# Kernel tuning notes

Measured on AMD Instinct MI355X. Metric: run time of the kernel, lower is better.

## Reference

```python
import jax, jax.numpy as jnp
import numpy as np

HEADS = 4
DIM_HEAD = 64
SCALE = 8.0
EPS = 1e-5  # fp32 branch of the original LayerNorm


def setup_inputs() -> dict:
    key = jax.random.key(0)
    k1, k2, k3 = jax.random.split(key, 3)
    B, C, F, H, W = 2, 256, 4, 32, 32
    inner = HEADS * DIM_HEAD  # 256
    x = jax.random.normal(k1, (B, C, F, H, W), dtype=jnp.float32)
    gamma = jnp.ones((1, C, 1, 1, 1), dtype=jnp.float32)
    w_qkv = jax.random.normal(k2, (3 * inner, C), dtype=jnp.float32) * 0.05
    w_out = jax.random.normal(k3, (C, inner), dtype=jnp.float32) * 0.05
    return {"x": x, "gamma": gamma, "w_qkv": w_qkv, "w_out": w_out}


def _l2norm(t):
    return t / jnp.sqrt(jnp.sum(t * t, axis=-1, keepdims=True) + 1e-12)


def reference(x, gamma, w_qkv, w_out):
    B, C, F, H, W = x.shape
    N = F * H * W
    inner = HEADS * DIM_HEAD
    residual = x

    # channel LayerNorm (biased variance over dim=1)
    mean = jnp.mean(x, axis=1, keepdims=True)
    var = jnp.mean((x - mean) ** 2, axis=1, keepdims=True)
    xn = (x - mean) / jnp.sqrt(var + EPS) * gamma

    # 1x1x1 conv == channel matmul; flatten spatial dims to sequence
    xn_flat = xn.reshape(B, C, N)                      # [B, C, N]
    qkv = jnp.einsum('oc,bcn->bon', w_qkv, xn_flat)    # [B, 3*inner, N]
    qkv = qkv.reshape(B, 3, HEADS, DIM_HEAD, N)        # chunk then split heads
    qkv = jnp.transpose(qkv, (1, 0, 2, 4, 3))          # [3, B, h, N, d]
    q, k, v = qkv[0], qkv[1], qkv[2]

    q = _l2norm(q)
    k = _l2norm(k)

    sim = jnp.einsum('bhid,bhjd->bhij', q, k) * SCALE  # [B, h, N, N]
    attn = jax.nn.softmax(sim, axis=-1)
    out = jnp.einsum('bhij,bhjd->bhid', attn, v)       # [B, h, N, d]

    # 'b h n d -> b (h d) n' then 1x1x1 out conv
    out = jnp.transpose(out, (0, 1, 3, 2)).reshape(B, inner, N)
    out = jnp.einsum('oi,bin->bon', w_out, out).reshape(B, C, F, H, W)
    return out + residual
```

## Files before the change

kernel.cpp:

```cpp
#include <hip/hip_runtime.h>

#define BATCH 2
#define CCH   256
#define NSEQ  4096
#define NH    4
#define DH    64
#define INNER 256

typedef __attribute__((ext_vector_type(8))) __bf16 bf16x8;
typedef __attribute__((ext_vector_type(4))) float f32x4;
typedef __attribute__((ext_vector_type(8))) unsigned short u16x8;
typedef __attribute__((ext_vector_type(4))) unsigned short u16x4;
typedef __attribute__((ext_vector_type(4))) short s16x4;

#define GLD16(gsrc, ldst)                                                     \
  __builtin_amdgcn_global_load_lds(                                           \
      (const __attribute__((address_space(1))) unsigned int*)(const void*)(gsrc), \
      (__attribute__((address_space(3))) unsigned int*)(void*)(ldst), 16, 0, 0)

static __device__ __forceinline__ unsigned short f2bfr(float f) {
  union { float f; unsigned u; } v; v.f = f;
  return (unsigned short)((v.u + 0x8000u) >> 16);
}
static __device__ __forceinline__ unsigned pack2(float f0, float f1) {
  union { float f; unsigned u; } a, b; a.f = f0; b.f = f1;
  return __builtin_amdgcn_perm(b.u + 0x8000u, a.u + 0x8000u, 0x07060302u);
}
static __device__ __forceinline__ float bf2f(unsigned short u) {
  union { unsigned u; float f; } v; v.u = ((unsigned)u) << 16;
  return v.f;
}
static __device__ __forceinline__ bf16x8 ldb(const unsigned short* p) {
  return *(const bf16x8*)p;
}
static __device__ __forceinline__ f32x4 mm(bf16x8 a, bf16x8 b, f32x4 c) {
  return __builtin_amdgcn_mfma_f32_16x16x32_bf16(a, b, c, 0, 0, 0);
}
static __device__ __forceinline__ f32x4 mm16(s16x4 a, s16x4 b, f32x4 c) {
  return __builtin_amdgcn_mfma_f32_16x16x16bf16_1k(a, b, c, 0, 0, 0);
}

__global__ __launch_bounds__(256) void k_lncvt(const float* __restrict__ x,
                                               const float* __restrict__ gamma,
                                               unsigned short* __restrict__ xn,
                                               const float* __restrict__ wq,
                                               const float* __restrict__ wo,
                                               unsigned short* __restrict__ wqb,
                                               unsigned short* __restrict__ wob) {
  int blk = blockIdx.x;
  if (blk >= 256) {
    int t = (blk - 256) * 256 + threadIdx.x;
    int e = t * 4;
    if (e < 768 * 256) {
      float4 v = *(const float4*)(wq + e);
      u16x4 pk = { f2bfr(v.x), f2bfr(v.y), f2bfr(v.z), f2bfr(v.w) };
      *(u16x4*)(wqb + e) = pk;
    } else {
      int e2 = e - 768 * 256;
      float4 v = *(const float4*)(wo + e2);
      u16x4 pk = { f2bfr(v.x), f2bfr(v.y), f2bfr(v.z), f2bfr(v.w) };
      *(u16x4*)(wob + e2) = pk;
    }
    return;
  }
  int b  = blk >> 7;
  int n0 = (blk & 127) * 32;
  int t  = threadIdx.x;
  int nl = t & 31;
  int cg = t >> 5;
  int n  = n0 + nl;
  const float* xp = x + ((size_t)(b * CCH + cg * 32)) * NSEQ + n;
  float vals[32];
  float s = 0.f, s2 = 0.f;
#pragma unroll
  for (int j = 0; j < 32; j++) {
    float v = xp[(size_t)j * NSEQ];
    vals[j] = v; s += v; s2 += v * v;
  }
  __shared__ float rs[8][32], rs2[8][32];
  rs[cg][nl] = s; rs2[cg][nl] = s2;
  __syncthreads();
  float S = 0.f, S2 = 0.f;
#pragma unroll
  for (int g = 0; g < 8; g++) { S += rs[g][nl]; S2 += rs2[g][nl]; }
  float mean = S * (1.f / 256.f);
  float var  = S2 * (1.f / 256.f) - mean * mean;
  float rstd = rsqrtf(var + 1e-5f);
  unsigned short* dst = xn + ((size_t)b * NSEQ + n) * CCH + cg * 32;
#pragma unroll
  for (int j0 = 0; j0 < 32; j0 += 8) {
    u16x8 pk;
#pragma unroll
    for (int j = 0; j < 8; j++)
      pk[j] = f2bfr((vals[j0 + j] - mean) * rstd * gamma[cg * 32 + j0 + j]);
    *(u16x8*)(dst + j0) = pk;
  }
}

__global__ __launch_bounds__(256) void k_qkv(const unsigned short* __restrict__ wqb,
                                             const unsigned short* __restrict__ xn,
                                             unsigned short* __restrict__ qkv,
                                             unsigned short* __restrict__ qt,
                                             unsigned short* __restrict__ ktb) {
  int n0 = blockIdx.x * 64;
  int oi = blockIdx.y;
  int o0 = oi * 64;
  int b  = blockIdx.z;
  __shared__ unsigned short Al[64 * 128];
  __shared__ unsigned short Bl[64 * 128];
  int t = threadIdx.x;
  int lane = t & 63, w = t >> 6;
  int c = lane & 15, quad = lane >> 4;
  int wm = w >> 1, wn = w & 1;
  f32x4 acc[2][2] = {};
  int lr = lane >> 4;
  int lchk = lane & 15;
  const unsigned short* apg = wqb + (size_t)o0 * CCH;
  const unsigned short* bpg = xn + ((size_t)b * NSEQ + n0) * CCH;
  for (int kt = 0; kt < 2; kt++) {
    if (kt) __syncthreads();
#pragma unroll
    for (int q = 0; q < 4; q++) {
      int r = w * 16 + q * 4 + lr;
      int srcoff = r * CCH + kt * 128 + ((lchk ^ (r & 7)) * 8);
      GLD16(apg + srcoff, Al + (size_t)(w * 16 + q * 4) * 128);
      GLD16(bpg + srcoff, Bl + (size_t)(w * 16 + q * 4) * 128);
    }
    __syncthreads();
#pragma unroll
    for (int ks = 0; ks < 4; ks++) {
      int ra0 = wm * 32 + c, ra1 = ra0 + 16;
      int rb0 = wn * 32 + c, rb1 = rb0 + 16;
      bf16x8 a0 = ldb(&Al[ra0 * 128 + (((ks * 4 + quad) ^ (ra0 & 7)) * 8)]);
      bf16x8 a1 = ldb(&Al[ra1 * 128 + (((ks * 4 + quad) ^ (ra1 & 7)) * 8)]);
      bf16x8 b0 = ldb(&Bl[rb0 * 128 + (((ks * 4 + quad) ^ (rb0 & 7)) * 8)]);
      bf16x8 b1 = ldb(&Bl[rb1 * 128 + (((ks * 4 + quad) ^ (rb1 & 7)) * 8)]);
      acc[0][0] = mm(a0, b0, acc[0][0]);
      acc[0][1] = mm(a0, b1, acc[0][1]);
      acc[1][0] = mm(a1, b0, acc[1][0]);
      acc[1][1] = mm(a1, b1, acc[1][1]);
    }
  }
  if (oi < 8) {
    float* sq = (float*)Al;
    float s0 = 0.f, s1 = 0.f;
#pragma unroll
    for (int i = 0; i < 2; i++)
#pragma unroll
      for (int rr = 0; rr < 4; rr++) {
        s0 += acc[i][0][rr] * acc[i][0][rr];
        s1 += acc[i][1][rr] * acc[i][1][rr];
      }
    s0 += __shfl_xor(s0, 16); s0 += __shfl_xor(s0, 32);
    s1 += __shfl_xor(s1, 16); s1 += __shfl_xor(s1, 32);
    __syncthreads();
    if (quad == 0) {
      sq[wm * 64 + wn * 32 + c]      = s0;
      sq[wm * 64 + wn * 32 + 16 + c] = s1;
    }
    __syncthreads();
    float r0 = rsqrtf(sq[wn * 32 + c]      + sq[64 + wn * 32 + c]      + 1e-12f);
    float r1 = rsqrtf(sq[wn * 32 + 16 + c] + sq[64 + wn * 32 + 16 + c] + 1e-12f);
    if (oi < 4) { r0 *= 11.541560327111707f; r1 *= 11.541560327111707f; }
    int h = oi & 3;
    unsigned short* base = (oi < 4 ? qt : ktb) + ((size_t)(b * NH + h) * NSEQ) * DH;
#pragma unroll
    for (int i = 0; i < 2; i++)
#pragma unroll
      for (int j = 0; j < 2; j++) {
        float rsc = j ? r1 : r0;
        int n = n0 + wn * 32 + j * 16 + c;
        int d = wm * 32 + i * 16 + quad * 4;
        uint2 pk = { pack2(acc[i][j][0] * rsc, acc[i][j][1] * rsc),
                     pack2(acc[i][j][2] * rsc, acc[i][j][3] * rsc) };
        *(uint2*)(base + (size_t)n * DH + d) = pk;
      }
  } else {
#pragma unroll
    for (int i = 0; i < 2; i++)
#pragma unroll
      for (int j = 0; j < 2; j++)
#pragma unroll
        for (int rr = 0; rr < 4; rr++) {
          int o = o0 + wm * 32 + i * 16 + quad * 4 + rr;
          int n = n0 + wn * 32 + j * 16 + c;
          qkv[((size_t)b * 768 + o) * NSEQ + n] = f2bfr(acc[i][j][rr]);
        }
  }
}

__global__ __launch_bounds__(256, 4) void k_attn(
    const unsigned short* __restrict__ qt,
    const unsigned short* __restrict__ ktb,
    const unsigned short* __restrict__ qkv,
    unsigned short* __restrict__ opart,
    float* __restrict__ lpart,
    int S, int kvlen) {
  int i0 = blockIdx.x * 128;
  int h  = blockIdx.y;
  int bz = blockIdx.z;
  int b  = bz / S, s = bz % S;
  __shared__ unsigned short Kl[2][64 * 64];
  __shared__ unsigned short Vl[2][64 * 64];
  int t = threadIdx.x;
  int lane = t & 63, w = t >> 6;
  int c = lane & 15, quad = lane >> 4;

  const unsigned short* qbase = qt  + ((size_t)(b * NH + h) * NSEQ) * DH;
  const unsigned short* kbase = ktb + ((size_t)(b * NH + h) * NSEQ) * DH;
  const unsigned short* vbase = qkv + ((size_t)b * 768 + 512 + h * 64) * NSEQ;

  int rlo = w * 32 + c, rhi = rlo + 16;
  const unsigned short* qlo = qbase + (size_t)(i0 + rlo) * DH + quad * 8;
  const unsigned short* qhi = qlo + 16 * DH;
  bf16x8 qlo0 = ldb(qlo), qlo1 = ldb(qlo + 32);
  bf16x8 qhi0 = ldb(qhi), qhi1 = ldb(qhi + 32);

  f32x4 acc[2][4] = {};
  float accl[2] = {0.f, 0.f};

  int slr = lane >> 3, slc = lane & 7;
  int ssw = (slc ^ slr) * 8;
  const unsigned short* kp = kbase + (size_t)(s * kvlen + w * 16 + slr) * DH + ssw;
  const unsigned short* vp = vbase + (size_t)(w * 16 + slr) * NSEQ + s * kvlen + ssw;
  int sw0 = (quad ^ (c & 7)) * 8;
  int sw1 = sw0 ^ 32;

  int nIt = kvlen / 64;
  GLD16(kp,            &Kl[0][(w * 16)     * 64]);
  GLD16(kp + 8 * DH,   &Kl[0][(w * 16 + 8) * 64]);
  GLD16(vp,            &Vl[0][(w * 16)     * 64]);
  GLD16(vp + 8 * NSEQ, &Vl[0][(w * 16 + 8) * 64]);
  kp += 64 * DH; vp += 64;

  for (int it = 0; it < nIt; it++) {
    int cur = it & 1;
    __syncthreads();
    if (it + 1 < nIt) {
      int nb = cur ^ 1;
      GLD16(kp,            &Kl[nb][(w * 16)     * 64]);
      GLD16(kp + 8 * DH,   &Kl[nb][(w * 16 + 8) * 64]);
      GLD16(vp,            &Vl[nb][(w * 16)     * 64]);
      GLD16(vp + 8 * NSEQ, &Vl[nb][(w * 16 + 8) * 64]);
      kp += 64 * DH; vp += 64;
    }

    s16x4 pf[2][4];
#pragma unroll
    for (int jt = 0; jt < 4; jt++) {
      bf16x8 k0 = ldb(&Kl[cur][(jt * 16 + c) * 64 + sw0]);
      bf16x8 k1 = ldb(&Kl[cur][(jt * 16 + c) * 64 + sw1]);
      f32x4 zl = {}; zl = mm(k0, qlo0, zl); zl = mm(k1, qlo1, zl);
      f32x4 zh = {}; zh = mm(k0, qhi0, zh); zh = mm(k1, qhi1, zh);
      float a0 = exp2f(zl[0]), a1 = exp2f(zl[1]),
            a2 = exp2f(zl[2]), a3 = exp2f(zl[3]);
      accl[0] += (a0 + a1) + (a2 + a3);
      uint2 pl = { pack2(a0, a1), pack2(a2, a3) };
      pf[0][jt] = *(s16x4*)&pl;
      float b0 = exp2f(zh[0]), b1 = exp2f(zh[1]),
            b2 = exp2f(zh[2]), b3 = exp2f(zh[3]);
      accl[1] += (b0 + b1) + (b2 + b3);
      uint2 ph = { pack2(b0, b1), pack2(b2, b3) };
      pf[1][jt] = *(s16x4*)&ph;
    }
#pragma unroll
    for (int dt = 0; dt < 4; dt++) {
      int row = dt * 16 + c;
      int rx = row & 7;
#pragma unroll
      for (int jt = 0; jt < 4; jt++) {
        int cj = jt * 2 + (quad >> 1);
        s16x4 a = *(const s16x4*)&Vl[cur][row * 64 + (((cj ^ rx) * 8) | ((quad & 1) * 4))];
        acc[0][dt] = mm16(a, pf[0][jt], acc[0][dt]);
        acc[1][dt] = mm16(a, pf[1][jt], acc[1][dt]);
      }
    }
  }

  accl[0] += __shfl_xor(accl[0], 16); accl[0] += __shfl_xor(accl[0], 32);
  accl[1] += __shfl_xor(accl[1], 16); accl[1] += __shfl_xor(accl[1], 32);

  size_t rb = ((size_t)(b * NH + h) * S + s) * NSEQ + i0 + w * 32;
  if (quad == 0) {
    lpart[rb + c]      = accl[0];
    lpart[rb + 16 + c] = accl[1];
  }
#pragma unroll
  for (int dt = 0; dt < 4; dt++) {
    uint2 p0 = { pack2(acc[0][dt][0], acc[0][dt][1]),
                 pack2(acc[0][dt][2], acc[0][dt][3]) };
    *(uint2*)&opart[(rb + c) * 64 + dt * 16 + quad * 4] = p0;
    uint2 p1 = { pack2(acc[1][dt][0], acc[1][dt][1]),
                 pack2(acc[1][dt][2], acc[1][dt][3]) };
    *(uint2*)&opart[(rb + 16 + c) * 64 + dt * 16 + quad * 4] = p1;
  }
}

__global__ __launch_bounds__(256) void k_merge(
    const unsigned short* __restrict__ opart,
    const float* __restrict__ lpart,
    unsigned short* __restrict__ ao, int S) {
  int t = blockIdx.x * 256 + threadIdx.x;
  int row = t >> 2;
  int dseg = (t & 3) * 16;
  int b = row >> 14, rem = row & 16383;
  int h = rem >> 12, i = rem & 4095;

  float l = 0.f;
  float o[16];
#pragma unroll
  for (int j = 0; j < 16; j++) o[j] = 0.f;
  for (int s = 0; s < S; s++) {
    size_t rb = ((size_t)(b * NH + h) * S + s) * NSEQ + i;
    l += lpart[rb];
    const unsigned short* p = opart + rb * 64 + dseg;
    u16x8 v0 = *(const u16x8*)p;
    u16x8 v1 = *(const u16x8*)(p + 8);
#pragma unroll
    for (int j = 0; j < 8; j++) {
      o[j]     += bf2f(v0[j]);
      o[8 + j] += bf2f(v1[j]);
    }
  }
  float inv = 1.f / l;
  unsigned short* dst = ao + ((size_t)b * NSEQ + i) * INNER + h * 64 + dseg;
  uint4 pk0 = { pack2(o[0] * inv, o[1] * inv),  pack2(o[2] * inv, o[3] * inv),
                pack2(o[4] * inv, o[5] * inv),  pack2(o[6] * inv, o[7] * inv) };
  uint4 pk1 = { pack2(o[8] * inv, o[9] * inv),  pack2(o[10] * inv, o[11] * inv),
                pack2(o[12] * inv, o[13] * inv),pack2(o[14] * inv, o[15] * inv) };
  *(uint4*)dst = pk0;
  *(uint4*)(dst + 8) = pk1;
}

__global__ __launch_bounds__(256) void k_out(const unsigned short* __restrict__ wob,
                                             const unsigned short* __restrict__ ao,
                                             const float* __restrict__ x,
                                             float* __restrict__ out) {
  int n0 = blockIdx.x * 64;
  int o0 = blockIdx.y * 64;
  int b  = blockIdx.z;
  __shared__ unsigned short Al[64 * 128];
  __shared__ unsigned short Bl[64 * 128];
  int t = threadIdx.x;
  int lane = t & 63, w = t >> 6;
  int c = lane & 15, quad = lane >> 4;
  int wm = w >> 1, wn = w & 1;
  f32x4 acc[2][2] = {};
  int lr = lane >> 4;
  int lchk = lane & 15;
  const unsigned short* apg = wob + (size_t)o0 * INNER;
  const unsigned short* bpg = ao + ((size_t)b * NSEQ + n0) * INNER;
  for (int kt = 0; kt < 2; kt++) {
    if (kt) __syncthreads();
#pragma unroll
    for (int q = 0; q < 4; q++) {
      int r = w * 16 + q * 4 + lr;
      int srcoff = r * INNER + kt * 128 + ((lchk ^ (r & 7)) * 8);
      GLD16(apg + srcoff, Al + (size_t)(w * 16 + q * 4) * 128);
      GLD16(bpg + srcoff, Bl + (size_t)(w * 16 + q * 4) * 128);
    }
    __syncthreads();
#pragma unroll
    for (int ks = 0; ks < 4; ks++) {
      int ra0 = wm * 32 + c, ra1 = ra0 + 16;
      int rb0 = wn * 32 + c, rb1 = rb0 + 16;
      bf16x8 a0 = ldb(&Al[ra0 * 128 + (((ks * 4 + quad) ^ (ra0 & 7)) * 8)]);
      bf16x8 a1 = ldb(&Al[ra1 * 128 + (((ks * 4 + quad) ^ (ra1 & 7)) * 8)]);
      bf16x8 b0 = ldb(&Bl[rb0 * 128 + (((ks * 4 + quad) ^ (rb0 & 7)) * 8)]);
      bf16x8 b1 = ldb(&Bl[rb1 * 128 + (((ks * 4 + quad) ^ (rb1 & 7)) * 8)]);
      acc[0][0] = mm(a0, b0, acc[0][0]);
      acc[0][1] = mm(a0, b1, acc[0][1]);
      acc[1][0] = mm(a1, b0, acc[1][0]);
      acc[1][1] = mm(a1, b1, acc[1][1]);
    }
  }
#pragma unroll
  for (int i = 0; i < 2; i++)
#pragma unroll
    for (int j = 0; j < 2; j++)
#pragma unroll
      for (int rr = 0; rr < 4; rr++) {
        int o = o0 + wm * 32 + i * 16 + quad * 4 + rr;
        int n = n0 + wn * 32 + j * 16 + c;
        size_t idx = ((size_t)b * CCH + o) * NSEQ + n;
        out[idx] = acc[i][j][rr] + x[idx];
      }
}

extern "C" void kernel_launch(void* const* d_in, const int* in_sizes, int n_in,
                              void* d_out, int out_size, void* d_ws, size_t ws_size,
                              hipStream_t stream) {
  const float* x     = (const float*)d_in[0];
  const float* gamma = (const float*)d_in[1];
  const float* wq    = (const float*)d_in[2];
  const float* wo    = (const float*)d_in[3];
  float* out = (float*)d_out;

  const size_t MB = 1u << 20;
  char* ws = (char*)d_ws;
  unsigned short* ao  = (unsigned short*)ws;
  unsigned short* xn  = (unsigned short*)(ws + 4 * MB);
  unsigned short* qkv = (unsigned short*)(ws + 8 * MB);
  unsigned short* wqb = (unsigned short*)(ws + 20 * MB);
  unsigned short* wob = (unsigned short*)(ws + 20 * MB + 512 * 1024);
  unsigned short* qt  = (unsigned short*)(ws + 21 * MB);
  unsigned short* ktb = (unsigned short*)(ws + 25 * MB);
  unsigned short* opart = (unsigned short*)(ws + 29 * MB);
  int S;
  if (ws_size >= 48 * MB) S = 4;
  else if (ws_size >= 40 * MB) S = 2;
  else S = 1;
  size_t opart_bytes = (size_t)S * BATCH * NH * NSEQ * DH * 2;
  float* lpart = (float*)(ws + 29 * MB + opart_bytes);
  int kvlen = NSEQ / S;

  k_lncvt<<<dim3(512),          256, 0, stream>>>(x, gamma, xn, wq, wo, wqb, wob);
  k_qkv  <<<dim3(64, 12, 2),    256, 0, stream>>>(wqb, xn, qkv, qt, ktb);
  k_attn <<<dim3(32, 4, 2 * S), 256, 0, stream>>>(qt, ktb, qkv, opart,
                                                  lpart, S, kvlen);
  k_merge<<<dim3(512),          256, 0, stream>>>(opart, lpart, ao, S);
  k_out  <<<dim3(64, 4, 2),     256, 0, stream>>>(wob, ao, x, out);
}
```

Baseline: 146.7 us.

## Single-buffer attention tiles, raise occupancy, MFMA row sums, deeper KV split

The attention kernel drops the double-buffered K/V LDS tiles in favour of single buffers with an extra barrier per tile. It raises the launch-bounds occupancy hint from 4 to 6 waves and computes softmax row sums with an MFMA against a ones vector, replacing the scalar adds and cross-lane shuffles. The workspace is compacted by writing only V into a dedicated per-head buffer, which lets the KV split factor go up to 8 when enough workspace exists. The aim is more parallelism and occupancy to hide latency, at the cost of losing load/compute overlap within a block and doing more merge work.

```diff
diff --git a/kernel.cpp b/kernel.cpp
--- a/kernel.cpp
+++ b/kernel.cpp
@@ -99,7 +99,7 @@
 
 __global__ __launch_bounds__(256) void k_qkv(const unsigned short* __restrict__ wqb,
                                              const unsigned short* __restrict__ xn,
-                                             unsigned short* __restrict__ qkv,
+                                             unsigned short* __restrict__ vtb,
                                              unsigned short* __restrict__ qt,
                                              unsigned short* __restrict__ ktb) {
   int n0 = blockIdx.x * 64;
@@ -176,23 +176,25 @@
         *(uint2*)(base + (size_t)n * DH + d) = pk;
       }
   } else {
+    int h = oi - 8;
+    unsigned short* vb = vtb + (size_t)(b * NH + h) * DH * NSEQ;
 #pragma unroll
     for (int i = 0; i < 2; i++)
 #pragma unroll
       for (int j = 0; j < 2; j++)
 #pragma unroll
         for (int rr = 0; rr < 4; rr++) {
-          int o = o0 + wm * 32 + i * 16 + quad * 4 + rr;
+          int d = wm * 32 + i * 16 + quad * 4 + rr;
           int n = n0 + wn * 32 + j * 16 + c;
-          qkv[((size_t)b * 768 + o) * NSEQ + n] = f2bfr(acc[i][j][rr]);
+          vb[(size_t)d * NSEQ + n] = f2bfr(acc[i][j][rr]);
         }
   }
 }
 
-__global__ __launch_bounds__(256, 4) void k_attn(
+__global__ __launch_bounds__(256, 6) void k_attn(
     const unsigned short* __restrict__ qt,
     const unsigned short* __restrict__ ktb,
-    const unsigned short* __restrict__ qkv,
+    const unsigned short* __restrict__ vtb,
     unsigned short* __restrict__ opart,
     float* __restrict__ lpart,
     int S, int kvlen) {
@@ -200,15 +202,15 @@
   int h  = blockIdx.y;
   int bz = blockIdx.z;
   int b  = bz / S, s = bz % S;
-  __shared__ unsigned short Kl[2][64 * 64];
-  __shared__ unsigned short Vl[2][64 * 64];
+  __shared__ unsigned short Kl[64 * 64];
+  __shared__ unsigned short Vl[64 * 64];
   int t = threadIdx.x;
   int lane = t & 63, w = t >> 6;
   int c = lane & 15, quad = lane >> 4;
 
   const unsigned short* qbase = qt  + ((size_t)(b * NH + h) * NSEQ) * DH;
   const unsigned short* kbase = ktb + ((size_t)(b * NH + h) * NSEQ) * DH;
-  const unsigned short* vbase = qkv + ((size_t)b * 768 + 512 + h * 64) * NSEQ;
+  const unsigned short* vbase = vtb + (size_t)(b * NH + h) * DH * NSEQ;
 
   int rlo = w * 32 + c, rhi = rlo + 16;
   const unsigned short* qlo = qbase + (size_t)(i0 + rlo) * DH + quad * 8;
@@ -216,8 +218,12 @@
   bf16x8 qlo0 = ldb(qlo), qlo1 = ldb(qlo + 32);
   bf16x8 qhi0 = ldb(qhi), qhi1 = ldb(qhi + 32);
 
+  s16x4 ones4;
+#pragma unroll
+  for (int j = 0; j < 4; j++) ones4[j] = (short)0x3F80;
+
   f32x4 acc[2][4] = {};
-  float accl[2] = {0.f, 0.f};
+  f32x4 accl[2] = {};
 
   int slr = lane >> 3, slc = lane & 7;
   int ssw = (slc ^ slr) * 8;
@@ -227,41 +233,30 @@
   int sw1 = sw0 ^ 32;
 
   int nIt = kvlen / 64;
-  GLD16(kp,            &Kl[0][(w * 16)     * 64]);
-  GLD16(kp + 8 * DH,   &Kl[0][(w * 16 + 8) * 64]);
-  GLD16(vp,            &Vl[0][(w * 16)     * 64]);
-  GLD16(vp + 8 * NSEQ, &Vl[0][(w * 16 + 8) * 64]);
-  kp += 64 * DH; vp += 64;
-
   for (int it = 0; it < nIt; it++) {
-    int cur = it & 1;
+    if (it) __syncthreads();
+    GLD16(kp,            &Kl[(w * 16)     * 64]);
+    GLD16(kp + 8 * DH,   &Kl[(w * 16 + 8) * 64]);
+    GLD16(vp,            &Vl[(w * 16)     * 64]);
+    GLD16(vp + 8 * NSEQ, &Vl[(w * 16 + 8) * 64]);
+    kp += 64 * DH; vp += 64;
     __syncthreads();
-    if (it + 1 < nIt) {
-      int nb = cur ^ 1;
-      GLD16(kp,            &Kl[nb][(w * 16)     * 64]);
-      GLD16(kp + 8 * DH,   &Kl[nb][(w * 16 + 8) * 64]);
-      GLD16(vp,            &Vl[nb][(w * 16)     * 64]);
-      GLD16(vp + 8 * NSEQ, &Vl[nb][(w * 16 + 8) * 64]);
-      kp += 64 * DH; vp += 64;
-    }
 
     s16x4 pf[2][4];
 #pragma unroll
     for (int jt = 0; jt < 4; jt++) {
-      bf16x8 k0 = ldb(&Kl[cur][(jt * 16 + c) * 64 + sw0]);
-      bf16x8 k1 = ldb(&Kl[cur][(jt * 16 + c) * 64 + sw1]);
+      bf16x8 k0 = ldb(&Kl[(jt * 16 + c) * 64 + sw0]);
+      bf16x8 k1 = ldb(&Kl[(jt * 16 + c) * 64 + sw1]);
       f32x4 zl = {}; zl = mm(k0, qlo0, zl); zl = mm(k1, qlo1, zl);
       f32x4 zh = {}; zh = mm(k0, qhi0, zh); zh = mm(k1, qhi1, zh);
-      float a0 = exp2f(zl[0]), a1 = exp2f(zl[1]),
-            a2 = exp2f(zl[2]), a3 = exp2f(zl[3]);
-      accl[0] += (a0 + a1) + (a2 + a3);
-      uint2 pl = { pack2(a0, a1), pack2(a2, a3) };
+      uint2 pl = { pack2(exp2f(zl[0]), exp2f(zl[1])),
+                   pack2(exp2f(zl[2]), exp2f(zl[3])) };
       pf[0][jt] = *(s16x4*)&pl;
-      float b0 = exp2f(zh[0]), b1 = exp2f(zh[1]),
-            b2 = exp2f(zh[2]), b3 = exp2f(zh[3]);
-      accl[1] += (b0 + b1) + (b2 + b3);
-      uint2 ph = { pack2(b0, b1), pack2(b2, b3) };
+      uint2 ph = { pack2(exp2f(zh[0]), exp2f(zh[1])),
+                   pack2(exp2f(zh[2]), exp2f(zh[3])) };
       pf[1][jt] = *(s16x4*)&ph;
+      accl[0] = mm16(ones4, pf[0][jt], accl[0]);
+      accl[1] = mm16(ones4, pf[1][jt], accl[1]);
     }
 #pragma unroll
     for (int dt = 0; dt < 4; dt++) {
@@ -270,20 +265,17 @@
 #pragma unroll
       for (int jt = 0; jt < 4; jt++) {
         int cj = jt * 2 + (quad >> 1);
-        s16x4 a = *(const s16x4*)&Vl[cur][row * 64 + (((cj ^ rx) * 8) | ((quad & 1) * 4))];
+        s16x4 a = *(const s16x4*)&Vl[row * 64 + (((cj ^ rx) * 8) | ((quad & 1) * 4))];
         acc[0][dt] = mm16(a, pf[0][jt], acc[0][dt]);
         acc[1][dt] = mm16(a, pf[1][jt], acc[1][dt]);
       }
     }
   }
 
-  accl[0] += __shfl_xor(accl[0], 16); accl[0] += __shfl_xor(accl[0], 32);
-  accl[1] += __shfl_xor(accl[1], 16); accl[1] += __shfl_xor(accl[1], 32);
-
   size_t rb = ((size_t)(b * NH + h) * S + s) * NSEQ + i0 + w * 32;
   if (quad == 0) {
-    lpart[rb + c]      = accl[0];
-    lpart[rb + 16 + c] = accl[1];
+    lpart[rb + c]      = accl[0][0];
+    lpart[rb + 16 + c] = accl[1][0];
   }
 #pragma unroll
   for (int dt = 0; dt < 4; dt++) {
@@ -400,23 +392,24 @@
   char* ws = (char*)d_ws;
   unsigned short* ao  = (unsigned short*)ws;
   unsigned short* xn  = (unsigned short*)(ws + 4 * MB);
-  unsigned short* qkv = (unsigned short*)(ws + 8 * MB);
-  unsigned short* wqb = (unsigned short*)(ws + 20 * MB);
-  unsigned short* wob = (unsigned short*)(ws + 20 * MB + 512 * 1024);
-  unsigned short* qt  = (unsigned short*)(ws + 21 * MB);
-  unsigned short* ktb = (unsigned short*)(ws + 25 * MB);
-  unsigned short* opart = (unsigned short*)(ws + 29 * MB);
+  unsigned short* vtb = (unsigned short*)(ws + 8 * MB);
+  unsigned short* wqb = (unsigned short*)(ws + 12 * MB);
+  unsigned short* wob = (unsigned short*)(ws + 12 * MB + 512 * 1024);
+  unsigned short* qt  = (unsigned short*)(ws + 13 * MB);
+  unsigned short* ktb = (unsigned short*)(ws + 17 * MB);
+  unsigned short* opart = (unsigned short*)(ws + 21 * MB);
   int S;
-  if (ws_size >= 48 * MB) S = 4;
-  else if (ws_size >= 40 * MB) S = 2;
+  if (ws_size >= 57 * MB) S = 8;
+  else if (ws_size >= 40 * MB) S = 4;
+  else if (ws_size >= 31 * MB) S = 2;
   else S = 1;
   size_t opart_bytes = (size_t)S * BATCH * NH * NSEQ * DH * 2;
-  float* lpart = (float*)(ws + 29 * MB + opart_bytes);
+  float* lpart = (float*)(ws + 21 * MB + opart_bytes);
   int kvlen = NSEQ / S;
 
   k_lncvt<<<dim3(512),          256, 0, stream>>>(x, gamma, xn, wq, wo, wqb, wob);
-  k_qkv  <<<dim3(64, 12, 2),    256, 0, stream>>>(wqb, xn, qkv, qt, ktb);
-  k_attn <<<dim3(32, 4, 2 * S), 256, 0, stream>>>(qt, ktb, qkv, opart,
+  k_qkv  <<<dim3(64, 12, 2),    256, 0, stream>>>(wqb, xn, vtb, qt, ktb);
+  k_attn <<<dim3(32, 4, 2 * S), 256, 0, stream>>>(qt, ktb, vtb, opart,
                                                   lpart, S, kvlen);
   k_merge<<<dim3(512),          256, 0, stream>>>(opart, lpart, ao, S);
   k_out  <<<dim3(64, 4, 2),     256, 0, stream>>>(wob, ao, x, out);
```

New measurement: 243.1 us. 65.7% more time.
